# Kernel tuning notes

Measured on AMD Instinct MI355X. Metric: run time of the kernel, lower is better.

Reference implementation:

```python
import jax, jax.numpy as jnp
import numpy as np

L, H, P = 32768, 256, 256
DT_MIN, DT_MAX = 0.001, 0.1


def setup_inputs() -> dict:
    key = jax.random.key(0)
    ks = jax.random.split(key, 7)
    signal = jax.random.normal(ks[0], (L, H), jnp.float32)
    # stable HiPPO-like init: negative real part, random imaginary part
    lam_re = -(0.1 + 0.4 * jax.random.uniform(ks[1], (P,), jnp.float32))
    lam_im = jax.random.normal(ks[2], (P,), jnp.float32)
    Lambda_ri = jnp.stack([lam_re, lam_im], axis=-1)            # (P, 2)
    B_ri = jax.random.normal(ks[3], (P, H, 2), jnp.float32) / np.float32(np.sqrt(H))
    C_ri = jax.random.normal(ks[4], (H, P, 2), jnp.float32) / np.float32(np.sqrt(P))
    D = jax.random.uniform(ks[5], (H,), jnp.float32)
    log_step = jnp.log(DT_MIN + (DT_MAX - DT_MIN) * jax.random.uniform(ks[6], (P,), jnp.float32))
    return {"signal": signal, "Lambda_ri": Lambda_ri, "B_ri": B_ri,
            "C_ri": C_ri, "D": D, "log_step": log_step}


def reference(signal, Lambda_ri, B_ri, C_ri, D, log_step):
    # --- get_BC_tilde (bcInit='dense'): B stored real (P,H,2) -> complex ---
    Lambda = jax.lax.complex(Lambda_ri[..., 0], Lambda_ri[..., 1])   # (P,)
    B_tilde = jax.lax.complex(B_ri[..., 0], B_ri[..., 1])            # (P, H)
    C_tilde = jax.lax.complex(C_ri[..., 0], C_ri[..., 1])            # (H, P)

    # --- discretize_zoh ---
    step = jnp.exp(log_step)                                          # (P,) step_scale = 1.0
    Lambda_bar = jnp.exp(Lambda * step)                               # (P,) complex
    B_bar = ((Lambda_bar - 1.0) / Lambda)[:, None] * B_tilde          # (P, H) complex

    # --- apply_ssm: Bu_elements = vmap(u -> B_bar @ u) over time ---
    Bu = signal.astype(Lambda_bar.dtype) @ B_bar.T                    # (L, P) complex
    Lam = jnp.broadcast_to(Lambda_bar, Bu.shape)                      # (L, P)

    def binop(qi, qj):
        A_i, Bu_i = qi
        A_j, Bu_j = qj
        return (A_j * A_i, Bu_j + A_j * Bu_i)

    _, xs = jax.lax.associative_scan(binop, (Lam, Bu), axis=0)        # (L, P)

    # y = Re(C_tilde @ x) + D * u, vectorized over time
    y = jnp.real(xs @ C_tilde.T) + D * signal                         # (L, H)
    return y
```

## Files before the change

kernel.cpp:

```cpp
#include <hip/hip_runtime.h>
#include <math.h>

constexpr int L = 32768;
constexpr int H = 256;
constexpr int P = 256;
constexpr int T = 64;
constexpr int NC = L / T;
constexpr int N1 = 2 * P;
constexpr int LDEP = 130;

typedef __attribute__((ext_vector_type(8))) short short8;
typedef __attribute__((ext_vector_type(4))) float f32x4;

__device__ __forceinline__ unsigned f2bf(float f) {
  unsigned u = __float_as_uint(f);
  return (u + 0x7FFFu + ((u >> 16) & 1u)) >> 16;
}

__device__ __forceinline__ void gload_lds16(const unsigned short* g, unsigned short* l) {
  __builtin_amdgcn_global_load_lds(
      (const __attribute__((address_space(1))) unsigned int*)(g),
      (__attribute__((address_space(3))) unsigned int*)(l), 16, 0, 0);
}

#define KBAR(N) do { \
    asm volatile("s_waitcnt vmcnt(" #N ") lgkmcnt(0)" ::: "memory"); \
    __builtin_amdgcn_s_barrier(); \
    __builtin_amdgcn_sched_barrier(0); \
  } while (0)

#define VMEM_FENCE() __builtin_amdgcn_sched_barrier(0x38F)

__device__ __forceinline__ void lambda_bar_of(const float* __restrict__ lam,
                                              const float* __restrict__ lstep,
                                              int p, float& lbr, float& lbi) {
  float lr = lam[2 * p], li = lam[2 * p + 1];
  float st = expf(lstep[p]);
  float ea = expf(lr * st);
  lbr = ea * cosf(li * st);
  lbi = ea * sinf(li * st);
}

__device__ __forceinline__ unsigned pkcm(float ar, float ai, float br, float bi) {
  float re = ar * br - ai * bi;
  float im = fmaf(ar, bi, ai * br);
  return f2bf(re) | (f2bf(im) << 16);
}

__global__ __launch_bounds__(256) void k_prep(const float* __restrict__ sig,
                                              const float* __restrict__ lam,
                                              const float* __restrict__ lstep,
                                              const float* __restrict__ Bri,
                                              const float* __restrict__ Cri,
                                              unsigned short* __restrict__ Bcat,
                                              unsigned short* __restrict__ Ccat,
                                              float* __restrict__ powc,
                                              unsigned short* __restrict__ sigt) {
  int idx = blockIdx.x * 256 + threadIdx.x;
  if (idx < N1 * H) {
    int n = idx >> 8, k = idx & 255;
    int p = n >> 1, comp = n & 1;
    float lr = lam[2 * p], li = lam[2 * p + 1];
    float st = expf(lstep[p]);
    float ea = expf(lr * st);
    float lbr = ea * cosf(li * st), lbi = ea * sinf(li * st);
    float inv = 1.0f / (lr * lr + li * li);
    float nr = lbr - 1.0f;
    float fr = (nr * lr + lbi * li) * inv;
    float fi = (lbi * lr - nr * li) * inv;
    float br = Bri[2 * (p * H + k)], bi = Bri[2 * (p * H + k) + 1];
    float v = (comp == 0) ? (fr * br - fi * bi) : (fr * bi + fi * br);
    Bcat[idx] = (unsigned short)f2bf(v);
  } else if (idx < 2 * N1 * H) {
    int j = idx - N1 * H;
    int h = j >> 9, k2 = j & 511;
    int p = k2 >> 1;
    float v = ((k2 & 1) == 0) ? Cri[2 * (h * P + p)] : -Cri[2 * (h * P + p) + 1];
    Ccat[j] = (unsigned short)f2bf(v);
  } else if (idx < 2 * N1 * H + T * P) {
    int r = idx - 2 * N1 * H;
    int t = r >> 8, p = r & 255;
    float lr = lam[2 * p], li = lam[2 * p + 1];
    float st = expf(lstep[p]);
    float e = (float)(t + 1);
    float er = expf(e * lr * st);
    powc[2 * r] = er * cosf(e * li * st);
    powc[2 * r + 1] = er * sinf(e * li * st);
  } else {
    int C = idx - (2 * N1 * H + T * P);
    int panel = C >> 12;
    int ks = (C >> 9) & 7;
    int c = C & 511;
    int row = ((c >> 8) << 6) + (((c >> 6) & 3) << 4) + (c & 15);
    int kk = ((c >> 4) & 3) << 3;
    const float* s = sig + (size_t)(panel * 128 + row) * 256 + ks * 32 + kk;
    float4 a = *(const float4*)(s);
    float4 b = *(const float4*)(s + 4);
    uint4 w;
    w.x = f2bf(a.x) | (f2bf(a.y) << 16);
    w.y = f2bf(a.z) | (f2bf(a.w) << 16);
    w.z = f2bf(b.x) | (f2bf(b.y) << 16);
    w.w = f2bf(b.z) | (f2bf(b.w) << 16);
    *(uint4*)(sigt + (size_t)C * 8) = w;
  }
}

__global__ __launch_bounds__(256, 4) void k_gemm1s(const unsigned short* __restrict__ sigt,
                                                   const unsigned short* __restrict__ Bcat,
                                                   const float* __restrict__ lam,
                                                   const float* __restrict__ lstep,
                                                   unsigned short* __restrict__ Xl,
                                                   float* __restrict__ Sr,
                                                   float* __restrict__ Si) {
  constexpr int NIT = 8;
  __shared__ __align__(16) char smem[40960];
  unsigned short* sA[3] = {(unsigned short*)smem, (unsigned short*)(smem + 8192),
                           (unsigned short*)(smem + 16384)};
  unsigned short* sB[2] = {(unsigned short*)(smem + 24576), (unsigned short*)(smem + 32768)};
  float* sEpi = (float*)smem;
  const int tid = threadIdx.x;
  const int lane = tid & 63;
  const int wave = tid >> 6;
  const int wc = (wave & 1) * 64;
  const int n0 = blockIdx.y * 128;
  const int brow = ((tid >> 6) << 4) | (tid & 15);
  const int bko = ((tid >> 4) & 3) * 8;
  const int hb = (wave & 1) * 2048;
  const int afb = (wave >> 1) * 256;
  const unsigned short* apan = sigt + (size_t)blockIdx.x * 32768;
  f32x4 acc[4][4];
#pragma unroll
  for (int i = 0; i < 4; i++)
#pragma unroll
    for (int j = 0; j < 4; j++) acc[i][j] = (f32x4){0.f, 0.f, 0.f, 0.f};

#define ISSUE_A1(ks, buf) { \
    gload_lds16(apan + (ks) * 4096 + tid * 8, sA[buf] + tid * 8); \
    gload_lds16(apan + (ks) * 4096 + 2048 + tid * 8, sA[buf] + 2048 + tid * 8); }
#define ISSUE_B1(ks, buf) { \
    gload_lds16(Bcat + (size_t)(n0 + brow) * 256 + (ks) * 32 + bko, sB[buf] + tid * 8); \
    gload_lds16(Bcat + (size_t)(n0 + 64 + brow) * 256 + (ks) * 32 + bko, sB[buf] + 2048 + tid * 8); }

  ISSUE_A1(0, 0);
  VMEM_FENCE();
  ISSUE_B1(0, 0);
  VMEM_FENCE();
  ISSUE_A1(1, 1);
  VMEM_FENCE();
  KBAR(2);
#pragma unroll
  for (int it = 0; it < NIT; it++) {
    if (it + 1 < NIT) ISSUE_B1(it + 1, (it + 1) & 1);
    VMEM_FENCE();
    if (it + 2 < NIT) ISSUE_A1(it + 2, (it + 2) % 3);
    VMEM_FENCE();
    const unsigned short* sAc = sA[it % 3];
    const unsigned short* sBc = sB[it & 1];
    short8 af[4], bfr[4];
#pragma unroll
    for (int i = 0; i < 4; i++) af[i] = *(const short8*)(sAc + (afb + i * 64 + lane) * 8);
#pragma unroll
    for (int j = 0; j < 4; j++) bfr[j] = *(const short8*)(sBc + hb + (j * 64 + lane) * 8);
#pragma unroll
    for (int i = 0; i < 4; i++)
#pragma unroll
      for (int j = 0; j < 4; j++)
        acc[i][j] = __builtin_amdgcn_mfma_f32_16x16x32_bf16(af[i], bfr[j], acc[i][j], 0, 0, 0);
    if (it + 1 < NIT) {
      if (it + 2 < NIT) { KBAR(2); } else { KBAR(0); }
    }
  }
  __syncthreads();

  const int crow = (lane >> 4) * 4, ccol = wc + (lane & 15);
#pragma unroll
  for (int half = 0; half < 2; half++) {
    if ((wave >> 1) == half) {
#pragma unroll
      for (int i = 0; i < 4; i++)
#pragma unroll
        for (int j = 0; j < 4; j++)
#pragma unroll
          for (int g = 0; g < 4; g++)
            sEpi[(crow + i * 16 + g) * LDEP + ccol + j * 16] = acc[i][j][g];
    }
    __syncthreads();
    if (tid < 64) {
      const int pl = tid;
      const int gp = (n0 >> 1) + pl;
      const int c = blockIdx.x * 2 + half;
      float lbr, lbi;
      lambda_bar_of(lam, lstep, gp, lbr, lbi);
      float xr = 0.f, xi = 0.f;
      const float* e = sEpi + 2 * pl;
      const int ks = blockIdx.y * 4 + (pl >> 4);
      const int kkb = (pl >> 2) & 3;
      unsigned short* xlb = Xl + (size_t)blockIdx.x * 65536 + ks * 4096 + 2 * (pl & 3);
      for (int tb = 0; tb < T; tb += 8) {
        float2 v[8];
#pragma unroll
        for (int u = 0; u < 8; u++) v[u] = *(const float2*)(e + (tb + u) * LDEP);
        unsigned ov[8];
#pragma unroll
        for (int u = 0; u < 8; u++) {
          float nr = fmaf(lbr, xr, fmaf(-lbi, xi, v[u].x));
          float ni = fmaf(lbr, xi, fmaf(lbi, xr, v[u].y));
          xr = nr; xi = ni;
          ov[u] = f2bf(xr) | (f2bf(xi) << 16);
        }
        const int cb0 = (half << 8) | (((tb >> 4) & 3) << 6) | (kkb << 4) | (tb & 15);
#pragma unroll
        for (int u = 0; u < 8; u++)
          *(unsigned*)(xlb + (cb0 + u) * 8) = ov[u];
      }
      Sr[(size_t)gp * NC + c] = xr;
      Si[(size_t)gp * NC + c] = xi;
    }
    __syncthreads();
  }
#undef ISSUE_A1
#undef ISSUE_B1
}

__global__ __launch_bounds__(64) void k_carry2(const float* __restrict__ lam,
                                               const float* __restrict__ lstep,
                                               const float* __restrict__ Sr,
                                               const float* __restrict__ Si,
                                               float* __restrict__ carc) {
  const int p = blockIdx.x;
  const int t = threadIdx.x;
  float lr = lam[2 * p], li = lam[2 * p + 1];
  float st = expf(lstep[p]);
  float eT = expf((float)T * lr * st);
  float lTr = eT * cosf((float)T * li * st);
  float lTi = eT * sinf((float)T * li * st);
  float vr[8], vi[8];
  {
    const float* srp = Sr + (size_t)p * NC + t * 8;
    const float* sip = Si + (size_t)p * NC + t * 8;
    float4 a0 = *(const float4*)(srp), a1 = *(const float4*)(srp + 4);
    float4 b0 = *(const float4*)(sip), b1 = *(const float4*)(sip + 4);
    vr[0] = a0.x; vr[1] = a0.y; vr[2] = a0.z; vr[3] = a0.w;
    vr[4] = a1.x; vr[5] = a1.y; vr[6] = a1.z; vr[7] = a1.w;
    vi[0] = b0.x; vi[1] = b0.y; vi[2] = b0.z; vi[3] = b0.w;
    vi[4] = b1.x; vi[5] = b1.y; vi[6] = b1.z; vi[7] = b1.w;
  }
  float Br = 0.f, Bi = 0.f;
#pragma unroll
  for (int u = 0; u < 8; u++) {
    float nr = fmaf(lTr, Br, fmaf(-lTi, Bi, vr[u]));
    float ni = fmaf(lTr, Bi, fmaf(lTi, Br, vi[u]));
    Br = nr; Bi = ni;
  }
  float e8 = expf(8.0f * (float)T * lr * st);
  float Ar = e8 * cosf(8.0f * (float)T * li * st);
  float Ai = e8 * sinf(8.0f * (float)T * li * st);
#pragma unroll
  for (int d = 1; d < 64; d <<= 1) {
    float Aor = __shfl_up(Ar, d), Aoi = __shfl_up(Ai, d);
    float Bor = __shfl_up(Br, d), Boi = __shfl_up(Bi, d);
    if (t >= d) {
      float nBr = Ar * Bor - Ai * Boi + Br;
      float nBi = Ar * Boi + Ai * Bor + Bi;
      float nAr = Aor * Ar - Aoi * Ai;
      float nAi = Aor * Ai + Aoi * Ar;
      Br = nBr; Bi = nBi; Ar = nAr; Ai = nAi;
    }
  }
  float cr = __shfl_up(Br, 1), ci = __shfl_up(Bi, 1);
  if (t == 0) { cr = 0.f; ci = 0.f; }
#pragma unroll
  for (int u = 0; u < 8; u++) {
    float2 w; w.x = cr; w.y = ci;
    *(float2*)(carc + 2 * ((size_t)(t * 8 + u) * P + p)) = w;
    float nr = fmaf(lTr, cr, fmaf(-lTi, ci, vr[u]));
    float ni = fmaf(lTr, ci, fmaf(lTi, cr, vi[u]));
    cr = nr; ci = ni;
  }
}

__global__ __launch_bounds__(256, 4) void k_gemm2c(const unsigned short* __restrict__ Xl,
                                                   const unsigned short* __restrict__ Ccat,
                                                   const float* __restrict__ powc,
                                                   const float* __restrict__ carc,
                                                   const float* __restrict__ sig,
                                                   const float* __restrict__ Dv,
                                                   float* __restrict__ out) {
  constexpr int NIT = 32;
  __shared__ __align__(16) char smem[32768];
  unsigned short* sA[3] = {(unsigned short*)smem, (unsigned short*)(smem + 8192),
                           (unsigned short*)(smem + 16384)};
  unsigned short* sB[2] = {(unsigned short*)(smem + 24576), (unsigned short*)(smem + 28672)};
  const int tid = threadIdx.x;
  const int lane = tid & 63;
  const int wave = tid >> 6;
  const int m0 = blockIdx.x * 128, n0 = blockIdx.y * 64;
  const int brow = (((tid >> 6) & 3) << 4) | (tid & 15);
  const int bko = ((tid >> 4) & 3) * 8;
  const int afb = (wave >> 1) * 256;
  const int bfb = (wave & 1) * 2;
  const unsigned short* apan = Xl + (size_t)blockIdx.x * 65536;
  const int t_ = (((tid >> 6) & 3) << 4) | (tid & 15);
  const int kk1 = ((tid >> 4) & 3) << 3;
  const float* pwB = powc + t_ * 512 + kk1;
  const float* c1B = carc + (size_t)(blockIdx.x * 2) * 512 + kk1;
  const float* c2B = c1B + 512;
  f32x4 acc[4][2];
#pragma unroll
  for (int i = 0; i < 4; i++)
#pragma unroll
    for (int j = 0; j < 2; j++) acc[i][j] = (f32x4){0.f, 0.f, 0.f, 0.f};

#define ISSUE_A2(ks, buf) { \
    gload_lds16(apan + (ks) * 4096 + tid * 8, sA[buf] + tid * 8); \
    gload_lds16(apan + (ks) * 4096 + 2048 + tid * 8, sA[buf] + 2048 + tid * 8); }
#define ISSUE_B2(ks, buf) { \
    gload_lds16(Ccat + (size_t)(n0 + brow) * 512 + (ks) * 32 + bko, sB[buf] + tid * 8); }

  float4 pa, pb, ca, cb, da, db;
#define LOAD_T(ks) { const int ko_ = (ks) * 32; \
    pa = *(const float4*)(pwB + ko_); pb = *(const float4*)(pwB + ko_ + 4); \
    ca = *(const float4*)(c1B + ko_); cb = *(const float4*)(c1B + ko_ + 4); \
    da = *(const float4*)(c2B + ko_); db = *(const float4*)(c2B + ko_ + 4); }
#define STAGE_FIX(buf) { \
    uint4 o1, o2; \
    o1.x = pkcm(pa.x, pa.y, ca.x, ca.y); \
    o1.y = pkcm(pa.z, pa.w, ca.z, ca.w); \
    o1.z = pkcm(pb.x, pb.y, cb.x, cb.y); \
    o1.w = pkcm(pb.z, pb.w, cb.z, cb.w); \
    o2.x = pkcm(pa.x, pa.y, da.x, da.y); \
    o2.y = pkcm(pa.z, pa.w, da.z, da.w); \
    o2.z = pkcm(pb.x, pb.y, db.x, db.y); \
    o2.w = pkcm(pb.z, pb.w, db.z, db.w); \
    unsigned short* dA_ = sA[buf]; \
    *(uint4*)(dA_ + tid * 8) = o1; \
    *(uint4*)(dA_ + 2048 + tid * 8) = o2; }

  ISSUE_A2(0, 0);
  VMEM_FENCE();
  ISSUE_B2(0, 0);
  VMEM_FENCE();
  ISSUE_A2(1, 1);
  VMEM_FENCE();
  KBAR(2);
#pragma unroll
  for (int it = 0; it < NIT; it++) {
    if (it >= 15 && it + 1 < NIT) LOAD_T((it + 1) & 15);
    VMEM_FENCE();
    if (it + 1 < NIT) ISSUE_B2((it + 1) & 15, (it + 1) & 1);
    VMEM_FENCE();
    if (it + 2 < 16) ISSUE_A2(it + 2, (it + 2) % 3);
    VMEM_FENCE();
    if (it >= 15 && it + 1 < NIT) STAGE_FIX((it + 1) % 3);
    const unsigned short* sAc = sA[it % 3];
    const unsigned short* sBc = sB[it & 1];
    short8 af[4], bfr[2];
#pragma unroll
    for (int i = 0; i < 4; i++) af[i] = *(const short8*)(sAc + (afb + i * 64 + lane) * 8);
#pragma unroll
    for (int j = 0; j < 2; j++) bfr[j] = *(const short8*)(sBc + ((bfb + j) * 64 + lane) * 8);
#pragma unroll
    for (int i = 0; i < 4; i++)
#pragma unroll
      for (int j = 0; j < 2; j++)
        acc[i][j] = __builtin_amdgcn_mfma_f32_16x16x32_bf16(af[i], bfr[j], acc[i][j], 0, 0, 0);
    if (it + 1 < NIT) {
      if (it + 2 < 16) { KBAR(2); }
      else { KBAR(0); }
    }
  }

  const int crow = (wave >> 1) * 64 + (lane >> 4) * 4;
  const int ccol = (wave & 1) * 32 + (lane & 15);
  float dcol[2];
#pragma unroll
  for (int j = 0; j < 2; j++) dcol[j] = Dv[n0 + ccol + j * 16];
#pragma unroll
  for (int i = 0; i < 4; i++)
#pragma unroll
    for (int j = 0; j < 2; j++) {
      int col = n0 + ccol + j * 16;
#pragma unroll
      for (int g = 0; g < 4; g++) {
        int row = m0 + crow + i * 16 + g;
        out[(size_t)row * H + col] = acc[i][j][g] + dcol[j] * sig[(size_t)row * H + col];
      }
    }
#undef ISSUE_A2
#undef ISSUE_B2
#undef LOAD_T
#undef STAGE_FIX
}

extern "C" void kernel_launch(void* const* d_in, const int* in_sizes, int n_in,
                              void* d_out, int out_size, void* d_ws, size_t ws_size,
                              hipStream_t stream) {
  const float* sig = (const float*)d_in[0];
  const float* lam = (const float*)d_in[1];
  const float* Bri = (const float*)d_in[2];
  const float* Cri = (const float*)d_in[3];
  const float* Dv  = (const float*)d_in[4];
  const float* lst = (const float*)d_in[5];
  float* out = (float*)d_out;

  unsigned short* Bcat = (unsigned short*)d_ws;
  unsigned short* Ccat = Bcat + (size_t)N1 * H;
  unsigned short* Xl   = Ccat + (size_t)H * N1;
  float* powc = (float*)(Xl + (size_t)L * N1);
  float* carc = powc + 2 * T * P;
  float* Sr   = carc + 2 * NC * P;
  float* Si   = Sr + NC * P;
  unsigned short* sigt = (unsigned short*)(Si + NC * P);

  k_prep<<<(2 * N1 * H + T * P + L * H / 8) / 256, 256, 0, stream>>>(
      sig, lam, lst, Bri, Cri, Bcat, Ccat, powc, sigt);
  dim3 g1(L / 128, N1 / 128);
  k_gemm1s<<<g1, 256, 0, stream>>>(sigt, Bcat, lam, lst, Xl, Sr, Si);
  k_carry2<<<P, 64, 0, stream>>>(lam, lst, Sr, Si, carc);
  dim3 g2(L / 128, H / 64);
  k_gemm2c<<<g2, 256, 0, stream>>>(Xl, Ccat, powc, carc, sig, Dv, out);
}
```

Measured before the change: 171.7 us.

## Fold chunk carry correction into local states, halving second GEMM's K dimension

The second GEMM used to run a K of 1024: the local chunk states plus a separate correction block built from the power times carry products. It now adds the carry correction straight into the bf16 local states in registers before staging them to LDS, so the GEMM runs K=512 with 16 iterations. The A operand now goes global to registers to LDS instead of using direct LDS loads, which raises register pressure and adds a second bf16 rounding of the summed state.

```diff
diff --git a/kernel.cpp b/kernel.cpp
--- a/kernel.cpp
+++ b/kernel.cpp
@@ -16,6 +16,8 @@
   unsigned u = __float_as_uint(f);
   return (u + 0x7FFFu + ((u >> 16) & 1u)) >> 16;
 }
+__device__ __forceinline__ float bf_lo(unsigned u) { return __uint_as_float(u << 16); }
+__device__ __forceinline__ float bf_hi(unsigned u) { return __uint_as_float(u & 0xFFFF0000u); }
 
 __device__ __forceinline__ void gload_lds16(const unsigned short* g, unsigned short* l) {
   __builtin_amdgcn_global_load_lds(
@@ -41,9 +43,9 @@
   lbi = ea * sinf(li * st);
 }
 
-__device__ __forceinline__ unsigned pkcm(float ar, float ai, float br, float bi) {
-  float re = ar * br - ai * bi;
-  float im = fmaf(ar, bi, ai * br);
+__device__ __forceinline__ unsigned mix1(unsigned u, float pr, float pi, float cr, float ci) {
+  float re = bf_lo(u) + (pr * cr - pi * ci);
+  float im = bf_hi(u) + (pr * ci + pi * cr);
   return f2bf(re) | (f2bf(im) << 16);
 }
 
@@ -279,18 +281,47 @@
   }
 }
 
-__global__ __launch_bounds__(256, 4) void k_gemm2c(const unsigned short* __restrict__ Xl,
+struct XTRegs {
+  uint4 x0, x1;
+  float4 p0, p1, c0, c1, d0, d1;
+};
+
+__device__ __forceinline__ void load_xt(const unsigned short* apan, const float* pwB,
+                                        const float* c1B, const float* c2B,
+                                        int ks, int tid, XTRegs& r) {
+  const int ko = ks * 32;
+  r.x0 = *(const uint4*)(apan + ks * 4096 + tid * 8);
+  r.x1 = *(const uint4*)(apan + ks * 4096 + 2048 + tid * 8);
+  r.p0 = *(const float4*)(pwB + ko);  r.p1 = *(const float4*)(pwB + ko + 4);
+  r.c0 = *(const float4*)(c1B + ko);  r.c1 = *(const float4*)(c1B + ko + 4);
+  r.d0 = *(const float4*)(c2B + ko);  r.d1 = *(const float4*)(c2B + ko + 4);
+}
+
+__device__ __forceinline__ void stage_fix(unsigned short* dA, int tid, const XTRegs& r) {
+  uint4 o1, o2;
+  o1.x = mix1(r.x0.x, r.p0.x, r.p0.y, r.c0.x, r.c0.y);
+  o1.y = mix1(r.x0.y, r.p0.z, r.p0.w, r.c0.z, r.c0.w);
+  o1.z = mix1(r.x0.z, r.p1.x, r.p1.y, r.c1.x, r.c1.y);
+  o1.w = mix1(r.x0.w, r.p1.z, r.p1.w, r.c1.z, r.c1.w);
+  o2.x = mix1(r.x1.x, r.p0.x, r.p0.y, r.d0.x, r.d0.y);
+  o2.y = mix1(r.x1.y, r.p0.z, r.p0.w, r.d0.z, r.d0.w);
+  o2.z = mix1(r.x1.z, r.p1.x, r.p1.y, r.d1.x, r.d1.y);
+  o2.w = mix1(r.x1.w, r.p1.z, r.p1.w, r.d1.z, r.d1.w);
+  *(uint4*)(dA + tid * 8) = o1;
+  *(uint4*)(dA + 2048 + tid * 8) = o2;
+}
+
+__global__ __launch_bounds__(256, 4) void k_gemm2v(const unsigned short* __restrict__ Xl,
                                                    const unsigned short* __restrict__ Ccat,
                                                    const float* __restrict__ powc,
                                                    const float* __restrict__ carc,
                                                    const float* __restrict__ sig,
                                                    const float* __restrict__ Dv,
                                                    float* __restrict__ out) {
-  constexpr int NIT = 32;
-  __shared__ __align__(16) char smem[32768];
-  unsigned short* sA[3] = {(unsigned short*)smem, (unsigned short*)(smem + 8192),
-                           (unsigned short*)(smem + 16384)};
-  unsigned short* sB[2] = {(unsigned short*)(smem + 24576), (unsigned short*)(smem + 28672)};
+  constexpr int NIT = 16;
+  __shared__ __align__(16) char smem[24576];
+  unsigned short* sA[2] = {(unsigned short*)smem, (unsigned short*)(smem + 8192)};
+  unsigned short* sB[2] = {(unsigned short*)(smem + 16384), (unsigned short*)(smem + 20480)};
   const int tid = threadIdx.x;
   const int lane = tid & 63;
   const int wave = tid >> 6;
@@ -311,48 +342,33 @@
 #pragma unroll
     for (int j = 0; j < 2; j++) acc[i][j] = (f32x4){0.f, 0.f, 0.f, 0.f};
 
-#define ISSUE_A2(ks, buf) { \
-    gload_lds16(apan + (ks) * 4096 + tid * 8, sA[buf] + tid * 8); \
-    gload_lds16(apan + (ks) * 4096 + 2048 + tid * 8, sA[buf] + 2048 + tid * 8); }
 #define ISSUE_B2(ks, buf) { \
     gload_lds16(Ccat + (size_t)(n0 + brow) * 512 + (ks) * 32 + bko, sB[buf] + tid * 8); }
 
-  float4 pa, pb, ca, cb, da, db;
-#define LOAD_T(ks) { const int ko_ = (ks) * 32; \
-    pa = *(const float4*)(pwB + ko_); pb = *(const float4*)(pwB + ko_ + 4); \
-    ca = *(const float4*)(c1B + ko_); cb = *(const float4*)(c1B + ko_ + 4); \
-    da = *(const float4*)(c2B + ko_); db = *(const float4*)(c2B + ko_ + 4); }
-#define STAGE_FIX(buf) { \
-    uint4 o1, o2; \
-    o1.x = pkcm(pa.x, pa.y, ca.x, ca.y); \
-    o1.y = pkcm(pa.z, pa.w, ca.z, ca.w); \
-    o1.z = pkcm(pb.x, pb.y, cb.x, cb.y); \
-    o1.w = pkcm(pb.z, pb.w, cb.z, cb.w); \
-    o2.x = pkcm(pa.x, pa.y, da.x, da.y); \
-    o2.y = pkcm(pa.z, pa.w, da.z, da.w); \
-    o2.z = pkcm(pb.x, pb.y, db.x, db.y); \
-    o2.w = pkcm(pb.z, pb.w, db.z, db.w); \
-    unsigned short* dA_ = sA[buf]; \
-    *(uint4*)(dA_ + tid * 8) = o1; \
-    *(uint4*)(dA_ + 2048 + tid * 8) = o2; }
-
-  ISSUE_A2(0, 0);
+  XTRegs ra, rb;
+
+  load_xt(apan, pwB, c1B, c2B, 0, tid, ra);
   VMEM_FENCE();
   ISSUE_B2(0, 0);
   VMEM_FENCE();
-  ISSUE_A2(1, 1);
-  VMEM_FENCE();
-  KBAR(2);
+  load_xt(apan, pwB, c1B, c2B, 1, tid, rb);
+  VMEM_FENCE();
+  stage_fix(sA[0], tid, ra);
+  KBAR(8);
 #pragma unroll
   for (int it = 0; it < NIT; it++) {
-    if (it >= 15 && it + 1 < NIT) LOAD_T((it + 1) & 15);
+    if (it + 1 < NIT) ISSUE_B2(it + 1, (it + 1) & 1);
     VMEM_FENCE();
-    if (it + 1 < NIT) ISSUE_B2((it + 1) & 15, (it + 1) & 1);
+    if (it + 2 < NIT) {
+      if (((it + 2) & 1) == 0) { load_xt(apan, pwB, c1B, c2B, it + 2, tid, ra); }
+      else                     { load_xt(apan, pwB, c1B, c2B, it + 2, tid, rb); }
+    }
     VMEM_FENCE();
-    if (it + 2 < 16) ISSUE_A2(it + 2, (it + 2) % 3);
-    VMEM_FENCE();
-    if (it >= 15 && it + 1 < NIT) STAGE_FIX((it + 1) % 3);
-    const unsigned short* sAc = sA[it % 3];
+    if (it + 1 < NIT) {
+      if (((it + 1) & 1) == 0) { stage_fix(sA[0], tid, ra); }
+      else                     { stage_fix(sA[1], tid, rb); }
+    }
+    const unsigned short* sAc = sA[it & 1];
     const unsigned short* sBc = sB[it & 1];
     short8 af[4], bfr[2];
 #pragma unroll
@@ -365,7 +381,7 @@
       for (int j = 0; j < 2; j++)
         acc[i][j] = __builtin_amdgcn_mfma_f32_16x16x32_bf16(af[i], bfr[j], acc[i][j], 0, 0, 0);
     if (it + 1 < NIT) {
-      if (it + 2 < 16) { KBAR(2); }
+      if (it + 2 < NIT) { KBAR(8); }
       else { KBAR(0); }
     }
   }
@@ -386,10 +402,7 @@
         out[(size_t)row * H + col] = acc[i][j][g] + dcol[j] * sig[(size_t)row * H + col];
       }
     }
-#undef ISSUE_A2
 #undef ISSUE_B2
-#undef LOAD_T
-#undef STAGE_FIX
 }
 
 extern "C" void kernel_launch(void* const* d_in, const int* in_sizes, int n_in,
@@ -418,5 +431,5 @@
   k_gemm1s<<<g1, 256, 0, stream>>>(sigt, Bcat, lam, lst, Xl, Sr, Si);
   k_carry2<<<P, 64, 0, stream>>>(lam, lst, Sr, Si, carc);
   dim3 g2(L / 128, H / 64);
-  k_gemm2c<<<g2, 256, 0, stream>>>(Xl, Ccat, powc, carc, sig, Dv, out);
-}
+  k_gemm2v<<<g2, 256, 0, stream>>>(Xl, Ccat, powc, carc, sig, Dv, out);
+}
```

After: 165.4 us. -3.6%, faster.
